# Performance work log

Measured on AMD Instinct MI355X. Metric: run time of the kernel, lower is better.

Reference implementation:

```python
import jax, jax.numpy as jnp
import numpy as np

EPS = 1e-5  # BatchNorm eps


def setup_inputs() -> dict:
    key = jax.random.key(0)
    ks = jax.random.split(key, 13)
    B, C, H, W = 8, 256, 64, 64
    Ci = 128
    s = 0.05
    return {
        "x": jax.random.normal(ks[0], (B, C, H, W), jnp.float32),
        "Wt": jax.random.normal(ks[1], (Ci, C), jnp.float32) * s,
        "bt": jax.random.normal(ks[2], (Ci,), jnp.float32) * s,
        "Wp": jax.random.normal(ks[3], (Ci, C), jnp.float32) * s,
        "bp": jax.random.normal(ks[4], (Ci,), jnp.float32) * s,
        "Wg": jax.random.normal(ks[5], (Ci, C), jnp.float32) * s,
        "bg": jax.random.normal(ks[6], (Ci,), jnp.float32) * s,
        "Wz": jax.random.normal(ks[7], (C, Ci), jnp.float32) * s,
        "bz": jax.random.normal(ks[8], (C,), jnp.float32) * s,
        "gamma": jax.random.normal(ks[9], (C,), jnp.float32) * s,
        "beta": jax.random.normal(ks[10], (C,), jnp.float32) * s,
        "rmean": jax.random.normal(ks[11], (C,), jnp.float32) * s,
        "rvar": jax.random.uniform(ks[12], (C,), jnp.float32, 0.5, 1.5),
    }


def reference(x, Wt, bt, Wp, bp, Wg, bg, Wz, bz, gamma, beta, rmean, rvar):
    B, C, H, W = x.shape
    N = H * W
    xf = x.reshape(B, C, N)                                  # [B,C,N]
    # 1x1 conv projections == channel GEMMs
    theta = jnp.einsum('oc,bcn->bno', Wt, xf) + bt           # [B,N,Ci]
    phi = jnp.einsum('oc,bcn->bon', Wp, xf) + bp[:, None]    # [B,Ci,N]
    g = jnp.einsum('oc,bcn->bno', Wg, xf) + bg               # [B,N,Ci]
    # single-head attention over all N=H*W positions
    attn = jax.nn.softmax(jnp.einsum('bnc,bcm->bnm', theta, phi), axis=-1)
    y = jnp.einsum('bnm,bmc->bnc', attn, g)                  # [B,N,Ci]
    # W_z: 1x1 conv + BatchNorm (eval mode: running stats) + residual
    z = jnp.einsum('oc,bnc->bon', Wz, y) + bz[:, None]       # [B,C,N]
    inv = gamma / jnp.sqrt(rvar + EPS)                       # [C]
    zn = (z - rmean[:, None]) * inv[:, None] + beta[:, None]
    return zn.reshape(B, C, H, W) + x
```

## Files before the change

kernel.cpp:

```cpp
#include <hip/hip_runtime.h>
#include <stdint.h>

typedef __attribute__((ext_vector_type(8))) short bf16x8;
typedef __attribute__((ext_vector_type(4))) float f32x4;
typedef __attribute__((ext_vector_type(16))) float f32x16;

__device__ __forceinline__ unsigned short f32_to_bf16(float f) {
  union { float f; uint32_t u; } v; v.f = f;
  uint32_t u = v.u;
  u += 0x7fffu + ((u >> 16) & 1u);
  return (unsigned short)(u >> 16);
}

__device__ __forceinline__ float bf16_to_f32(unsigned short s) {
  union { uint32_t u; float f; } v; v.u = ((uint32_t)s) << 16;
  return v.f;
}

__device__ __forceinline__ uint32_t cvt_pk_bf16(float a, float b) {
  uint32_t r;
  asm("v_cvt_pk_bf16_f32 %0, %1, %2" : "=v"(r) : "v"(a), "v"(b));
  return r;
}

__device__ __forceinline__ void async_copy16(void* lds, const void* g) {
  __builtin_amdgcn_global_load_lds(
      (const __attribute__((address_space(1))) unsigned int*)g,
      (__attribute__((address_space(3))) unsigned int*)lds, 16, 0, 0);
}

__global__ __launch_bounds__(256) void xpose_kernel(
    const float* __restrict__ x, unsigned short* __restrict__ xT,
    unsigned short* __restrict__ xc) {
  __shared__ unsigned short ts[32][260];
  const int t = threadIdx.x;
  const int bid = blockIdx.x;
  const int b = bid >> 7;
  const int ct = (bid >> 4) & 7;
  const int nt = bid & 15;
  const int c0 = ct * 32, n0 = nt * 256;

  const float* xb = x + ((size_t)b * 256 + c0) * 4096 + n0;
#pragma unroll
  for (int i = 0; i < 8; ++i) {
    int flat = i * 256 + t;
    int c = flat >> 6, nq = flat & 63;
    float4 v = *(const float4*)(xb + (size_t)c * 4096 + nq * 4);
    union { uint2 u; unsigned short s[4]; } pk;
    pk.s[0] = f32_to_bf16(v.x); pk.s[1] = f32_to_bf16(v.y);
    pk.s[2] = f32_to_bf16(v.z); pk.s[3] = f32_to_bf16(v.w);
    *(uint2*)&ts[c][nq * 4] = pk.u;
    *(uint2*)(xc + ((size_t)b * 256 + c0 + c) * 4096 + n0 + nq * 4) = pk.u;
  }
  __syncthreads();

  unsigned short* xo = xT + ((size_t)b * 4096 + n0) * 256 + c0;
#pragma unroll
  for (int i = 0; i < 4; ++i) {
    int flat = i * 256 + t;
    int n = flat >> 2, ch = flat & 3;
    union { uint4 u; unsigned short s[8]; } pk;
#pragma unroll
    for (int jj = 0; jj < 8; ++jj) pk.s[jj] = ts[ch * 8 + jj][n];
    *(uint4*)(xo + (size_t)n * 256 + ch * 8) = pk.u;
  }
}

__global__ __launch_bounds__(256) void wcvt_kernel(
    const float* __restrict__ Wt, const float* __restrict__ Wp,
    const float* __restrict__ Wg, const float* __restrict__ Wz,
    unsigned short* __restrict__ Wcat, unsigned short* __restrict__ Wzb) {
  int e = (blockIdx.x * 256 + threadIdx.x) * 4;
  const float* src;
  unsigned short* dst;
  int off;
  if (e < 32768) { src = Wt; dst = Wcat; off = e; }
  else if (e < 65536) { src = Wp; dst = Wcat + 32768; off = e - 32768; }
  else if (e < 98304) { src = Wg; dst = Wcat + 65536; off = e - 65536; }
  else { src = Wz; dst = Wzb; off = e - 98304; }
  float4 v = *(const float4*)(src + off);
  union { uint2 u; unsigned short s[4]; } pk;
  pk.s[0] = f32_to_bf16(v.x); pk.s[1] = f32_to_bf16(v.y);
  pk.s[2] = f32_to_bf16(v.z); pk.s[3] = f32_to_bf16(v.w);
  *(uint2*)(dst + off) = pk.u;
}

__global__ __launch_bounds__(512, 2) void proj_kernel(
    const unsigned short* __restrict__ xT,
    const unsigned short* __restrict__ Wcat,
    const float* __restrict__ bt, const float* __restrict__ bp,
    const float* __restrict__ bg,
    unsigned short* __restrict__ Q, unsigned short* __restrict__ Km,
    unsigned short* __restrict__ Vt) {
  __shared__ __align__(1024) unsigned short xs[128 * 256];
  const int t = threadIdx.x;
  const int lane = t & 63;
  const int w = t >> 6;
  const int nt = blockIdx.x;
  const int b = blockIdx.y;
  const int n0 = nt * 128;

  const unsigned char* xTb =
      (const unsigned char*)(xT + ((size_t)b * 4096 + n0) * 256);
  unsigned char* lbase = (unsigned char*)xs;
#pragma unroll
  for (int i = 0; i < 8; ++i) {
    int base = (w * 8 + i) * 1024;
    int off = base + lane * 16;
    int n = off >> 9;
    int bir = off & 511;
    async_copy16(lbase + base, xTb + n * 512 + (bir ^ ((n & 7) << 4)));
  }
  __syncthreads();

  const int rl = lane & 15, gh = lane >> 4;
  const int swz = (rl & 7) << 4;
  const int rlv = (rl & 3) | ((rl & 4) << 1) | ((rl & 8) >> 1);

  f32x4 aQ[8], aK[8], aV[8];
#pragma unroll
  for (int i = 0; i < 8; ++i) {
    aQ[i] = (f32x4){0.f, 0.f, 0.f, 0.f};
    aK[i] = (f32x4){0.f, 0.f, 0.f, 0.f};
    aV[i] = (f32x4){0.f, 0.f, 0.f, 0.f};
  }

  const unsigned char* wq =
      (const unsigned char*)Wcat + ((w * 16 + rl) * 256) * 2 + gh * 16;
  const unsigned char* wk = wq + 128 * 512;
  const unsigned char* wv = wq + 256 * 512;

#pragma unroll
  for (int kk = 0; kk < 8; ++kk) {
    bf16x8 xf[8];
#pragma unroll
    for (int n2 = 0; n2 < 8; ++n2)
      xf[n2] = *(const bf16x8*)(lbase + (n2 * 16 + rl) * 512 +
                                ((kk * 64 + gh * 16) ^ swz));
    bf16x8 fq = *(const bf16x8*)(wq + kk * 64);
    bf16x8 fk = *(const bf16x8*)(wk + kk * 64);
    bf16x8 fv = *(const bf16x8*)(wv + kk * 64);
#pragma unroll
    for (int n2 = 0; n2 < 8; ++n2) {
      aQ[n2] = __builtin_amdgcn_mfma_f32_16x16x32_bf16(xf[n2], fq, aQ[n2], 0, 0, 0);
      aK[n2] = __builtin_amdgcn_mfma_f32_16x16x32_bf16(xf[n2], fk, aK[n2], 0, 0, 0);
      aV[n2] = __builtin_amdgcn_mfma_f32_16x16x32_bf16(fv, xf[n2], aV[n2], 0, 0, 0);
    }
  }

  const float btv = bt[w * 16 + rl];
  const float bpv = bp[w * 16 + rl];
  float bgv[4];
#pragma unroll
  for (int j = 0; j < 4; ++j) bgv[j] = bg[w * 16 + gh * 4 + j];

  unsigned short* Qb = Q + ((size_t)b * 4096 + n0) * 128 + w * 16 + rl;
  unsigned short* Kb = Km + ((size_t)b * 4096 + n0) * 128 + w * 16 + rl;
  unsigned short* Vb = Vt + (size_t)b * 128 * 4096 + n0 + rlv;
#pragma unroll
  for (int n2 = 0; n2 < 8; ++n2) {
#pragma unroll
    for (int j = 0; j < 4; ++j) {
      int n = n2 * 16 + gh * 4 + j;
      Qb[(size_t)n * 128] = f32_to_bf16(aQ[n2][j] + btv);
      Kb[(size_t)n * 128] = f32_to_bf16(aK[n2][j] + bpv);
      int o = w * 16 + gh * 4 + j;
      Vb[(size_t)o * 4096 + n2 * 16] = f32_to_bf16(aV[n2][j] + bgv[j]);
    }
  }
}

__global__ __launch_bounds__(256, 2) void attn_kernel(
    const unsigned short* __restrict__ Qg,
    const unsigned short* __restrict__ Kg,
    const unsigned short* __restrict__ Vg,
    unsigned short* __restrict__ Opart,
    float* __restrict__ Marr, float* __restrict__ Larr) {
  __shared__ __align__(1024) unsigned char smem[65536];
  const int t = threadIdx.x;
  const int lane = t & 63;
  const int w = t >> 6;
  const int q31 = lane & 31;
  const int hi = lane >> 5;
  const int kswz = (q31 & 15) << 4;

  const int orig = blockIdx.x;
  const int b = orig & 7;
  const int idx = orig >> 3;
  const int h = idx & 1;
  const int qg = idx >> 1;
  const int qw = qg * 128 + w * 32;
  const int kv0 = h * 2048;

  const unsigned short* Qb = Qg + (size_t)b * 4096 * 128;
  const unsigned short* Kb = Kg + (size_t)b * 4096 * 128;
  const unsigned short* Vb = Vg + (size_t)b * 128 * 4096;

  bf16x8 qf[8];
  {
    const unsigned char* qp =
        (const unsigned char*)(Qb + (size_t)(qw + q31) * 128) + hi * 16;
#pragma unroll
    for (int dc = 0; dc < 8; ++dc) qf[dc] = *(const bf16x8*)(qp + dc * 32);
  }

  const unsigned char* ksrc[4];
  const unsigned char* vsrc[4];
  unsigned int kofs[4], vofs[4];
#pragma unroll
  for (int ii = 0; ii < 4; ++ii) {
    int seg = w * 4 + ii;
    {
      int r = seg * 4 + (lane >> 4);
      int kcol = ((lane & 15) * 16) ^ ((r & 15) << 4);
      ksrc[ii] = (const unsigned char*)(Kb + (size_t)(kv0 + r) * 128) + kcol;
      kofs[ii] = seg * 1024;
    }
    {
      int o = seg * 1024 + lane * 16;
      int R = o >> 8;
      int cp = (o & 255) ^ ((R & 15) << 4);
      int d = 2 * R + (cp >> 7);
      int kvb = cp & 127;
      vsrc[ii] = (const unsigned char*)(Vb + (size_t)d * 4096 + kv0) + kvb;
      vofs[ii] = 16384 + seg * 1024;
    }
  }

  f32x16 acc[4];
#pragma unroll
  for (int i = 0; i < 4; ++i)
#pragma unroll
    for (int e = 0; e < 16; ++e) acc[i][e] = 0.f;
  float m = -1e30f, l = 0.f;

#pragma unroll
  for (int ii = 0; ii < 4; ++ii) {
    async_copy16(smem + kofs[ii], ksrc[ii]);
    async_copy16(smem + vofs[ii], vsrc[ii]);
  }
  __syncthreads();

#pragma unroll 2
  for (int it = 0; it < 32; ++it) {
    unsigned char* bb = smem + (it & 1) * 32768;
    if (it + 1 < 32) {
      unsigned int nb = ((it + 1) & 1) * 32768;
      size_t ko = (size_t)(it + 1) * 16384;
      int vo2 = (it + 1) * 128;
#pragma unroll
      for (int ii = 0; ii < 4; ++ii) {
        async_copy16(smem + nb + kofs[ii], ksrc[ii] + ko);
        async_copy16(smem + nb + vofs[ii], vsrc[ii] + vo2);
      }
    }

    f32x16 st0, st1;
#pragma unroll
    for (int e = 0; e < 16; ++e) { st0[e] = 0.f; st1[e] = 0.f; }
    const unsigned char* kb0 = bb + q31 * 256;
    const unsigned char* kb1 = bb + (32 + q31) * 256;
    __builtin_amdgcn_s_setprio(1);
#pragma unroll
    for (int dc = 0; dc < 8; ++dc) {
      int off = (dc * 32 + hi * 16) ^ kswz;
      bf16x8 k0 = *(const bf16x8*)(kb0 + off);
      bf16x8 k1 = *(const bf16x8*)(kb1 + off);
      st0 = __builtin_amdgcn_mfma_f32_32x32x16_bf16(k0, qf[dc], st0, 0, 0, 0);
      st1 = __builtin_amdgcn_mfma_f32_32x32x16_bf16(k1, qf[dc], st1, 0, 0, 0);
    }
    __builtin_amdgcn_s_setprio(0);

    float tmax = st0[0];
#pragma unroll
    for (int e = 1; e < 16; ++e) tmax = fmaxf(tmax, st0[e]);
#pragma unroll
    for (int e = 0; e < 16; ++e) tmax = fmaxf(tmax, st1[e]);
#pragma unroll
    for (int off = 1; off < 64; off <<= 1)
      tmax = fmaxf(tmax, __shfl_xor(tmax, off));
    if (tmax > m + 8.f) {
      float mn = fmaxf(m, tmax);
      float sc = __expf(m - mn);
      m = mn;
      l *= sc;
#pragma unroll
      for (int i = 0; i < 4; ++i)
#pragma unroll
        for (int e = 0; e < 16; ++e) acc[i][e] *= sc;
    }
    float ls = 0.f;
#pragma unroll
    for (int e = 0; e < 16; ++e) { st0[e] = __expf(st0[e] - m); ls += st0[e]; }
#pragma unroll
    for (int e = 0; e < 16; ++e) { st1[e] = __expf(st1[e] - m); ls += st1[e]; }
    l += ls;

    const unsigned char* vbase = bb + 16384 + (q31 >> 1) * 256;
    const int vhb = (q31 & 1) << 7;
    const int vswz = (q31 >> 1) << 4;
#pragma unroll
    for (int ks = 0; ks < 4; ++ks) {
      union { uint32_t u[4]; bf16x8 v; } pk;
      if (ks == 0) {
        pk.u[0] = cvt_pk_bf16(st0[0], st0[1]);
        pk.u[1] = cvt_pk_bf16(st0[2], st0[3]);
        pk.u[2] = cvt_pk_bf16(st0[4], st0[5]);
        pk.u[3] = cvt_pk_bf16(st0[6], st0[7]);
      } else if (ks == 1) {
        pk.u[0] = cvt_pk_bf16(st0[8], st0[9]);
        pk.u[1] = cvt_pk_bf16(st0[10], st0[11]);
        pk.u[2] = cvt_pk_bf16(st0[12], st0[13]);
        pk.u[3] = cvt_pk_bf16(st0[14], st0[15]);
      } else if (ks == 2) {
        pk.u[0] = cvt_pk_bf16(st1[0], st1[1]);
        pk.u[1] = cvt_pk_bf16(st1[2], st1[3]);
        pk.u[2] = cvt_pk_bf16(st1[4], st1[5]);
        pk.u[3] = cvt_pk_bf16(st1[6], st1[7]);
      } else {
        pk.u[0] = cvt_pk_bf16(st1[8], st1[9]);
        pk.u[1] = cvt_pk_bf16(st1[10], st1[11]);
        pk.u[2] = cvt_pk_bf16(st1[12], st1[13]);
        pk.u[3] = cvt_pk_bf16(st1[14], st1[15]);
      }
      __builtin_amdgcn_s_setprio(1);
#pragma unroll
      for (int dt = 0; dt < 4; ++dt) {
        bf16x8 vf = *(const bf16x8*)(
            vbase + dt * 4096 + ((vhb | (ks * 32 + hi * 16)) ^ vswz));
        acc[dt] = __builtin_amdgcn_mfma_f32_32x32x16_bf16(pk.v, vf, acc[dt], 0, 0, 0);
      }
      __builtin_amdgcn_s_setprio(0);
    }
    __syncthreads();
  }

  float lf = l + __shfl_xor(l, 32);
  if (lane < 32) {
    size_t ix = (size_t)h * 32768 + (size_t)b * 4096 + qw + q31;
    Marr[ix] = m;
    Larr[ix] = lf;
  }
  unsigned short* ob = Opart + (size_t)h * 32768 * 128;
#pragma unroll
  for (int dt = 0; dt < 4; ++dt)
#pragma unroll
    for (int r = 0; r < 16; ++r) {
      int qrow = qw + (r & 3) + 8 * (r >> 2) + 4 * hi;
      ob[((size_t)b * 4096 + qrow) * 128 + dt * 32 + q31] =
          f32_to_bf16(acc[dt][r]);
    }
}

__global__ __launch_bounds__(256) void comb_kernel(
    const unsigned short* __restrict__ Opart,
    const float* __restrict__ Marr, const float* __restrict__ Larr,
    unsigned short* __restrict__ Y) {
  int i = blockIdx.x * 256 + threadIdx.x;
  int q = i >> 4;
  int d8 = (i & 15) * 8;
  float m0 = Marr[q], m1 = Marr[32768 + q];
  float l0 = Larr[q], l1 = Larr[32768 + q];
  float M = fmaxf(m0, m1);
  float e0 = __expf(m0 - M), e1 = __expf(m1 - M);
  float rl = 1.f / (e0 * l0 + e1 * l1);
  float f0 = e0 * rl, f1 = e1 * rl;
  const bf16x8 o0 = *(const bf16x8*)(Opart + (size_t)q * 128 + d8);
  const bf16x8 o1 =
      *(const bf16x8*)(Opart + 32768ull * 128 + (size_t)q * 128 + d8);
  union { uint4 u4; unsigned short s[8]; } pk;
#pragma unroll
  for (int e = 0; e < 8; ++e) {
    float v = f0 * bf16_to_f32((unsigned short)o0[e]) +
              f1 * bf16_to_f32((unsigned short)o1[e]);
    pk.s[e] = f32_to_bf16(v);
  }
  *(uint4*)(Y + (size_t)q * 128 + d8) = pk.u4;
}

__global__ __launch_bounds__(512, 2) void outz_kernel(
    const unsigned short* __restrict__ Y,
    const unsigned short* __restrict__ Wzb,
    const unsigned short* __restrict__ xc, const float* __restrict__ bz,
    const float* __restrict__ gamma, const float* __restrict__ beta,
    const float* __restrict__ rmean, const float* __restrict__ rvar,
    float* __restrict__ out) {
  __shared__ __align__(1024) unsigned short ys[128 * 128];
  const int t = threadIdx.x;
  const int lane = t & 63;
  const int w = t >> 6;
  const int nt = blockIdx.x;
  const int b = blockIdx.y;
  const int n0 = nt * 128;

  const unsigned char* Yb =
      (const unsigned char*)(Y + ((size_t)b * 4096 + n0) * 128);
  unsigned char* lbase = (unsigned char*)ys;
#pragma unroll
  for (int i = 0; i < 4; ++i) {
    int base = (w * 4 + i) * 1024;
    int off = base + lane * 16;
    int n = off >> 8;
    int bir = off & 255;
    async_copy16(lbase + base, Yb + n * 256 + (bir ^ ((n & 7) << 4)));
  }
  __syncthreads();

  const int rl = lane & 15, gh = lane >> 4;
  const int swz = (rl & 7) << 4;

  f32x4 acc[2][8];
#pragma unroll
  for (int i = 0; i < 2; ++i)
#pragma unroll
    for (int j = 0; j < 8; ++j) acc[i][j] = (f32x4){0.f, 0.f, 0.f, 0.f};

  const unsigned char* wz0 =
      (const unsigned char*)Wzb + ((w * 2) * 16 + rl) * 256 + gh * 16;

#pragma unroll
  for (int kk = 0; kk < 4; ++kk) {
    bf16x8 yf[8];
#pragma unroll
    for (int n2 = 0; n2 < 8; ++n2)
      yf[n2] = *(const bf16x8*)(lbase + (n2 * 16 + rl) * 256 +
                                ((kk * 64 + gh * 16) ^ swz));
    bf16x8 f0 = *(const bf16x8*)(wz0 + kk * 64);
    bf16x8 f1 = *(const bf16x8*)(wz0 + 16 * 256 + kk * 64);
#pragma unroll
    for (int n2 = 0; n2 < 8; ++n2) {
      acc[0][n2] = __builtin_amdgcn_mfma_f32_16x16x32_bf16(f0, yf[n2], acc[0][n2], 0, 0, 0);
      acc[1][n2] = __builtin_amdgcn_mfma_f32_16x16x32_bf16(f1, yf[n2], acc[1][n2], 0, 0, 0);
    }
  }

#pragma unroll
  for (int ot = 0; ot < 2; ++ot) {
#pragma unroll
    for (int j = 0; j < 4; ++j) {
      int o = (w * 2 + ot) * 16 + gh * 4 + j;
      float scale = gamma[o] * rsqrtf(rvar[o] + 1e-5f);
      float shift = (bz[o] - rmean[o]) * scale + beta[o];
      const unsigned short* xr = xc + ((size_t)b * 256 + o) * 4096 + n0;
      float* orow = out + ((size_t)b * 256 + o) * 4096 + n0;
#pragma unroll
      for (int n2 = 0; n2 < 8; ++n2) {
        int n = n2 * 16 + rl;
        orow[n] = acc[ot][n2][j] * scale + shift + bf16_to_f32(xr[n]);
      }
    }
  }
}

extern "C" void kernel_launch(void* const* d_in, const int* in_sizes, int n_in,
                              void* d_out, int out_size, void* d_ws,
                              size_t ws_size, hipStream_t stream) {
  const float* x     = (const float*)d_in[0];
  const float* Wt    = (const float*)d_in[1];
  const float* bt    = (const float*)d_in[2];
  const float* Wp    = (const float*)d_in[3];
  const float* bp    = (const float*)d_in[4];
  const float* Wg    = (const float*)d_in[5];
  const float* bg    = (const float*)d_in[6];
  const float* Wz    = (const float*)d_in[7];
  const float* bz    = (const float*)d_in[8];
  const float* gamma = (const float*)d_in[9];
  const float* beta  = (const float*)d_in[10];
  const float* rmean = (const float*)d_in[11];
  const float* rvar  = (const float*)d_in[12];
  float* out = (float*)d_out;

  const size_t NE = (size_t)8 * 4096 * 128;
  unsigned short* Wcat  = (unsigned short*)d_ws;
  unsigned short* Wzb   = Wcat + 98304;
  float*          Marr  = (float*)(Wzb + 32768);
  float*          Larr  = Marr + 2 * 32768;
  unsigned short* xT    = (unsigned short*)(Larr + 2 * 32768);
  unsigned short* Q     = xT + 2 * NE;
  unsigned short* Km    = Q + NE;
  unsigned short* Vt    = Km + NE;
  unsigned short* xc    = Vt + NE;
  unsigned short* Opart = xT;
  unsigned short* Y     = Km;

  wcvt_kernel<<<128, 256, 0, stream>>>(Wt, Wp, Wg, Wz, Wcat, Wzb);
  xpose_kernel<<<1024, 256, 0, stream>>>(x, xT, xc);
  proj_kernel<<<dim3(32, 8), 512, 0, stream>>>(xT, Wcat, bt, bp, bg, Q, Km, Vt);
  attn_kernel<<<512, 256, 0, stream>>>(Q, Km, Vt, Opart, Marr, Larr);
  comb_kernel<<<2048, 256, 0, stream>>>(Opart, Marr, Larr, Y);
  outz_kernel<<<dim3(32, 8), 512, 0, stream>>>(Y, Wzb, xc, bz, gamma, beta,
                                               rmean, rvar, out);
}
```

Measured before the change: 137.9 us.

## Template attention split-KV count, shrink LDS to single V buffer for higher occupancy

Makes the attention kernel's KV split count a template parameter and uses a 4-way split (1024 blocks) when the workspace is large enough, with a generalized combine kernel. Shared memory drops from 64KB to 48KB by single-buffering V (loaded at iteration start, with an extra __syncthreads before the PV stage) while K stays double-buffered, and launch bounds rise to 3 blocks per CU. The goal is more parallelism and occupancy, traded against an extra barrier per iteration, less latency hiding for V, and more partial-output traffic in the combine step.

```diff
diff --git a/kernel.cpp b/kernel.cpp
--- a/kernel.cpp
+++ b/kernel.cpp
@@ -170,13 +170,16 @@
   }
 }
 
-__global__ __launch_bounds__(256, 2) void attn_kernel(
+template <int LOGSPLIT>
+__global__ __launch_bounds__(256, 3) void attn_kernel(
     const unsigned short* __restrict__ Qg,
     const unsigned short* __restrict__ Kg,
     const unsigned short* __restrict__ Vg,
     unsigned short* __restrict__ Opart,
     float* __restrict__ Marr, float* __restrict__ Larr) {
-  __shared__ __align__(1024) unsigned char smem[65536];
+  constexpr int NSPLIT = 1 << LOGSPLIT;
+  constexpr int ITERS = (4096 / NSPLIT) / 64;
+  __shared__ __align__(1024) unsigned char smem[49152];
   const int t = threadIdx.x;
   const int lane = t & 63;
   const int w = t >> 6;
@@ -187,10 +190,10 @@
   const int orig = blockIdx.x;
   const int b = orig & 7;
   const int idx = orig >> 3;
-  const int h = idx & 1;
-  const int qg = idx >> 1;
+  const int h = idx & (NSPLIT - 1);
+  const int qg = idx >> LOGSPLIT;
   const int qw = qg * 128 + w * 32;
-  const int kv0 = h * 2048;
+  const int kv0 = h * (4096 / NSPLIT);
 
   const unsigned short* Qb = Qg + (size_t)b * 4096 * 128;
   const unsigned short* Kb = Kg + (size_t)b * 4096 * 128;
@@ -223,7 +226,7 @@
       int d = 2 * R + (cp >> 7);
       int kvb = cp & 127;
       vsrc[ii] = (const unsigned char*)(Vb + (size_t)d * 4096 + kv0) + kvb;
-      vofs[ii] = 16384 + seg * 1024;
+      vofs[ii] = 32768 + seg * 1024;
     }
   }
 
@@ -241,18 +244,20 @@
   }
   __syncthreads();
 
-#pragma unroll 2
-  for (int it = 0; it < 32; ++it) {
-    unsigned char* bb = smem + (it & 1) * 32768;
-    if (it + 1 < 32) {
-      unsigned int nb = ((it + 1) & 1) * 32768;
+  for (int it = 0; it < ITERS; ++it) {
+    unsigned char* bb = smem + (it & 1) * 16384;
+    if (it > 0) {
+      int vo2 = it * 128;
+#pragma unroll
+      for (int ii = 0; ii < 4; ++ii)
+        async_copy16(smem + vofs[ii], vsrc[ii] + vo2);
+    }
+    if (it + 1 < ITERS) {
+      unsigned int nb = ((it + 1) & 1) * 16384;
       size_t ko = (size_t)(it + 1) * 16384;
-      int vo2 = (it + 1) * 128;
-#pragma unroll
-      for (int ii = 0; ii < 4; ++ii) {
+#pragma unroll
+      for (int ii = 0; ii < 4; ++ii)
         async_copy16(smem + nb + kofs[ii], ksrc[ii] + ko);
-        async_copy16(smem + nb + vofs[ii], vsrc[ii] + vo2);
-      }
     }
 
     f32x16 st0, st1;
@@ -296,7 +301,9 @@
     for (int e = 0; e < 16; ++e) { st1[e] = __expf(st1[e] - m); ls += st1[e]; }
     l += ls;
 
-    const unsigned char* vbase = bb + 16384 + (q31 >> 1) * 256;
+    __syncthreads();
+
+    const unsigned char* vbase = smem + 32768 + (q31 >> 1) * 256;
     const int vhb = (q31 & 1) << 7;
     const int vswz = (q31 >> 1) << 4;
 #pragma unroll
@@ -352,6 +359,7 @@
     }
 }
 
+template <int NSPLIT>
 __global__ __launch_bounds__(256) void comb_kernel(
     const unsigned short* __restrict__ Opart,
     const float* __restrict__ Marr, const float* __restrict__ Larr,
@@ -359,22 +367,36 @@
   int i = blockIdx.x * 256 + threadIdx.x;
   int q = i >> 4;
   int d8 = (i & 15) * 8;
-  float m0 = Marr[q], m1 = Marr[32768 + q];
-  float l0 = Larr[q], l1 = Larr[32768 + q];
-  float M = fmaxf(m0, m1);
-  float e0 = __expf(m0 - M), e1 = __expf(m1 - M);
-  float rl = 1.f / (e0 * l0 + e1 * l1);
-  float f0 = e0 * rl, f1 = e1 * rl;
-  const bf16x8 o0 = *(const bf16x8*)(Opart + (size_t)q * 128 + d8);
-  const bf16x8 o1 =
-      *(const bf16x8*)(Opart + 32768ull * 128 + (size_t)q * 128 + d8);
+  float mv[NSPLIT], lv[NSPLIT];
+  float M = -1e30f;
+#pragma unroll
+  for (int s = 0; s < NSPLIT; ++s) {
+    mv[s] = Marr[s * 32768 + q];
+    lv[s] = Larr[s * 32768 + q];
+    M = fmaxf(M, mv[s]);
+  }
+  float fs[NSPLIT];
+  float denom = 0.f;
+#pragma unroll
+  for (int s = 0; s < NSPLIT; ++s) {
+    fs[s] = __expf(mv[s] - M);
+    denom += fs[s] * lv[s];
+  }
+  float rd = 1.f / denom;
+  float o[8];
+#pragma unroll
+  for (int e = 0; e < 8; ++e) o[e] = 0.f;
+#pragma unroll
+  for (int s = 0; s < NSPLIT; ++s) {
+    const bf16x8 os =
+        *(const bf16x8*)(Opart + (size_t)s * 32768 * 128 + (size_t)q * 128 + d8);
+#pragma unroll
+    for (int e = 0; e < 8; ++e)
+      o[e] += fs[s] * bf16_to_f32((unsigned short)os[e]);
+  }
   union { uint4 u4; unsigned short s[8]; } pk;
 #pragma unroll
-  for (int e = 0; e < 8; ++e) {
-    float v = f0 * bf16_to_f32((unsigned short)o0[e]) +
-              f1 * bf16_to_f32((unsigned short)o1[e]);
-    pk.s[e] = f32_to_bf16(v);
-  }
+  for (int e = 0; e < 8; ++e) pk.s[e] = f32_to_bf16(o[e] * rd);
   *(uint4*)(Y + (size_t)q * 128 + d8) = pk.u4;
 }
 
@@ -474,20 +496,29 @@
   unsigned short* Wcat  = (unsigned short*)d_ws;
   unsigned short* Wzb   = Wcat + 98304;
   float*          Marr  = (float*)(Wzb + 32768);
-  float*          Larr  = Marr + 2 * 32768;
-  unsigned short* xT    = (unsigned short*)(Larr + 2 * 32768);
+  float*          Larr  = Marr + 4 * 32768;
+  unsigned short* xT    = (unsigned short*)(Larr + 4 * 32768);
   unsigned short* Q     = xT + 2 * NE;
   unsigned short* Km    = Q + NE;
   unsigned short* Vt    = Km + NE;
   unsigned short* xc    = Vt + NE;
-  unsigned short* Opart = xT;
+  unsigned short* Obig  = xc + 2 * NE;
   unsigned short* Y     = Km;
+
+  const size_t need4 = (size_t)((char*)(Obig + 4 * NE) - (char*)d_ws);
+  const bool big = ws_size >= need4;
 
   wcvt_kernel<<<128, 256, 0, stream>>>(Wt, Wp, Wg, Wz, Wcat, Wzb);
   xpose_kernel<<<1024, 256, 0, stream>>>(x, xT, xc);
   proj_kernel<<<dim3(32, 8), 512, 0, stream>>>(xT, Wcat, bt, bp, bg, Q, Km, Vt);
-  attn_kernel<<<512, 256, 0, stream>>>(Q, Km, Vt, Opart, Marr, Larr);
-  comb_kernel<<<2048, 256, 0, stream>>>(Opart, Marr, Larr, Y);
+  if (big) {
+    attn_kernel<2><<<1024, 256, 0, stream>>>(Q, Km, Vt, Obig, Marr, Larr);
+    comb_kernel<4><<<2048, 256, 0, stream>>>(Obig, Marr, Larr, Y);
+  } else {
+    unsigned short* Opart = xT;
+    attn_kernel<1><<<512, 256, 0, stream>>>(Q, Km, Vt, Opart, Marr, Larr);
+    comb_kernel<2><<<2048, 256, 0, stream>>>(Opart, Marr, Larr, Y);
+  }
   outz_kernel<<<dim3(32, 8), 512, 0, stream>>>(Y, Wzb, xc, bz, gamma, beta,
                                                rmean, rvar, out);
 }
```

Result: slower. 331.2 us (+140.1%).
